# Performance work log

Hardware: AMD Instinct MI355X
Metric: run time of the kernel (lower is better)

The kernel has to match this reference:

```python
import jax, jax.numpy as jnp
import numpy as np

N_HEAD = 8
N_FEAT = 512
EPS = 1e-6


def _forward(query, Wq, bq, Wk, bk, Wv, bv, Wo, bo):
    # query: (bsz, tgt_len, E). key = value = query (self-attention).
    bsz, tgt_len, E = query.shape
    head_dim = E // N_HEAD
    n = bsz * N_HEAD

    # Faithful to torch: .view((L, N, E)) is a RESHAPE, not a transpose.
    x = query.reshape(tgt_len, bsz, E)

    q = x @ Wq.T + bq
    k = x @ Wk.T + bk
    v = x @ Wv.T + bv

    # relu activation on q, k (act_fun='relu')
    q = jax.nn.relu(q).reshape(tgt_len, n, head_dim).swapaxes(0, 1)  # (n, L, d)
    k = jax.nn.relu(k).reshape(tgt_len, n, head_dim).swapaxes(0, 1)  # (n, L, d)
    v = v.reshape(tgt_len, n, head_dim).swapaxes(0, 1)               # (n, L, d)

    # cos reweighting: weight_index = pi/2 * arange(1, m+1) / m
    m = tgt_len
    idx = (np.pi / 2) * jnp.arange(1, m + 1, dtype=query.dtype) / m  # (L,)
    idx = idx[None, :, None]                                         # (1, L, 1)
    q_ = jnp.concatenate([q * jnp.sin(idx), q * jnp.cos(idx)], axis=-1)  # (n, L, 2d)
    k_ = jnp.concatenate([k * jnp.sin(idx), k * jnp.cos(idx)], axis=-1)  # (n, L, 2d)

    # causal linear attention via cumsum recurrence
    kv = jnp.einsum('nld,nlm->nldm', k_, v)          # (n, L, 2d, d)
    kv_cum = jnp.cumsum(kv, axis=1)                  # (n, L, 2d, d)
    qkv = jnp.einsum('nld,nldm->nlm', q_, kv_cum)    # (n, L, d)
    k_cum = jnp.cumsum(k_, axis=1)                   # (n, L, 2d)
    denom = jnp.clip(jnp.einsum('nld,nld->nl', q_, k_cum), EPS, None)
    attn = qkv / denom[..., None]                    # (n, L, d)

    attn = attn.swapaxes(0, 1).reshape(tgt_len, bsz, E)
    out = attn @ Wo.T + bo
    # Faithful to torch: final .view back to (bsz, tgt_len, E) is a reshape.
    return out.reshape(bsz, tgt_len, N_FEAT)


def setup_inputs() -> dict:
    key = jax.random.key(0)
    ks = jax.random.split(key, 9)
    bsz, L, E = 2, 1024, N_FEAT
    scale = 0.02
    return {
        'query': jax.random.normal(ks[0], (bsz, L, E), dtype=jnp.float32),
        'Wq': jax.random.normal(ks[1], (E, E), dtype=jnp.float32) * scale,
        'bq': jnp.zeros((E,), dtype=jnp.float32),
        'Wk': jax.random.normal(ks[2], (E, E), dtype=jnp.float32) * scale,
        'bk': jnp.zeros((E,), dtype=jnp.float32),
        'Wv': jax.random.normal(ks[3], (E, E), dtype=jnp.float32) * scale,
        'bv': jnp.zeros((E,), dtype=jnp.float32),
        'Wo': jax.random.normal(ks[4], (E, E), dtype=jnp.float32) * scale,
        'bo': jnp.zeros((E,), dtype=jnp.float32),
    }


def reference(query, Wq, bq, Wk, bk, Wv, bv, Wo, bo):
    return _forward(query, Wq, bq, Wk, bk, Wv, bv, Wo, bo)
```

## Files before the change

kernel.cpp:

```cpp
#include <hip/hip_runtime.h>
#include <math.h>

#define LSEQ 1024
#define EDIM 512
#define HD 64
#define CCH 32
#define NCH 32
#define DFEAT 128

typedef unsigned short u16;
typedef short bf16x8 __attribute__((ext_vector_type(8)));
typedef float f32x4 __attribute__((ext_vector_type(4)));

__device__ __forceinline__ u16 f2bf(float f) {
    unsigned u = __float_as_uint(f);
    unsigned r = (u + 0x7fffu + ((u >> 16) & 1u)) >> 16;
    return (u16)r;
}
__device__ __forceinline__ float bf2f(u16 x) {
    return __uint_as_float((unsigned)x << 16);
}
__device__ __forceinline__ void async16(void* lds, const void* g) {
    __builtin_amdgcn_global_load_lds(
        (const __attribute__((address_space(1))) unsigned int*)g,
        (__attribute__((address_space(3))) unsigned int*)lds, 16, 0, 0);
}

__global__ __launch_bounds__(256) void cast_kernel(
    const float* __restrict__ X,  const float* __restrict__ Wq,
    const float* __restrict__ Wk, const float* __restrict__ Wv,
    const float* __restrict__ Wo, u16* __restrict__ Xb, u16* __restrict__ Wb)
{
    int i = blockIdx.x * 256 + threadIdx.x;
    const float* src; u16* dst; int off;
    if (i < 262144)      { src = X;  dst = Xb;          off = i; }
    else if (i < 327680) { src = Wq; dst = Wb;          off = i - 262144; }
    else if (i < 393216) { src = Wk; dst = Wb + 262144; off = i - 327680; }
    else if (i < 458752) { src = Wv; dst = Wb + 524288; off = i - 393216; }
    else                 { src = Wo; dst = Wb + 786432; off = i - 458752; }
    float4 v = *(const float4*)&src[(size_t)off * 4];
    ushort4 o; o.x = f2bf(v.x); o.y = f2bf(v.y); o.z = f2bf(v.z); o.w = f2bf(v.w);
    *(ushort4*)&dst[(size_t)off * 4] = o;
}

__global__ __launch_bounds__(256) void qkv_mfma_kernel(
    const u16* __restrict__ Xb, const u16* __restrict__ Wb,
    const float* __restrict__ bq, const float* __restrict__ bk, const float* __restrict__ bv,
    u16* __restrict__ qf, u16* __restrict__ kf, u16* __restrict__ vf)
{
    const int z = blockIdx.z;
    const u16* __restrict__ W = Wb + (size_t)z * 262144;
    const float* __restrict__ bias = (z == 0) ? bq : (z == 1) ? bk : bv;
    const int r0 = blockIdx.x * 128;
    const int j0 = blockIdx.y * 64;
    __shared__ u16 As[128 * 32];
    __shared__ u16 Bs[64 * 32];
    const int t = threadIdx.x;
    const int wave = t >> 6, lane = t & 63;
    const int cl = lane & 15, rg4 = lane >> 4;
    f32x4 acc[2][4];
    #pragma unroll
    for (int ri = 0; ri < 2; ++ri)
        #pragma unroll
        for (int cj = 0; cj < 4; ++cj) acc[ri][cj] = (f32x4){0.f, 0.f, 0.f, 0.f};

    for (int kb = 0; kb < 512; kb += 32) {
        #pragma unroll
        for (int i = 0; i < 2; ++i) {
            int chunk = i * 256 + t;
            int row = chunk >> 2, kg = chunk & 3;
            async16(&As[(i * 256 + wave * 64) * 8], Xb + (size_t)(r0 + row) * 512 + kb + kg * 8);
        }
        {
            int row = t >> 2, kg = t & 3;
            async16(&Bs[(wave * 64) * 8], W + (size_t)(j0 + row) * 512 + kb + kg * 8);
        }
        __syncthreads();
        bf16x8 af[2], bg[4];
        #pragma unroll
        for (int ri = 0; ri < 2; ++ri)
            af[ri] = *(const bf16x8*)&As[(wave * 32 + ri * 16 + cl) * 32 + rg4 * 8];
        #pragma unroll
        for (int cj = 0; cj < 4; ++cj)
            bg[cj] = *(const bf16x8*)&Bs[(cj * 16 + cl) * 32 + rg4 * 8];
        #pragma unroll
        for (int ri = 0; ri < 2; ++ri)
            #pragma unroll
            for (int cj = 0; cj < 4; ++cj)
                acc[ri][cj] = __builtin_amdgcn_mfma_f32_16x16x32_bf16(af[ri], bg[cj], acc[ri][cj], 0, 0, 0);
        __syncthreads();
    }

    float biasv[4];
    #pragma unroll
    for (int cj = 0; cj < 4; ++cj) biasv[cj] = bias[j0 + cj * 16 + cl];
    const int h = j0 >> 6;
    #pragma unroll
    for (int ri = 0; ri < 2; ++ri) {
        #pragma unroll
        for (int rr = 0; rr < 4; ++rr) {
            const int row_g = r0 + wave * 32 + ri * 16 + rg4 * 4 + rr;
            const int l = row_g >> 1, bb = row_g & 1;
            if (z < 2) {
                float ang = 1.5707963267948966f * (float)(l + 1) * (1.0f / 1024.0f);
                float sv, cv;
                sincosf(ang, &sv, &cv);
                u16* __restrict__ dst = (z == 0) ? qf : kf;
                size_t base = (size_t)((bb * 8 + h) * LSEQ + l) * DFEAT;
                #pragma unroll
                for (int cj = 0; cj < 4; ++cj) {
                    const int d = cj * 16 + cl;
                    float y = fmaxf(acc[ri][cj][rr] + biasv[cj], 0.f);
                    dst[base + d]      = f2bf(y * sv);
                    dst[base + d + 64] = f2bf(y * cv);
                }
            } else {
                size_t base = (size_t)((bb * 8 + h) * LSEQ + l) * HD;
                #pragma unroll
                for (int cj = 0; cj < 4; ++cj) {
                    const int d = cj * 16 + cl;
                    vf[base + d] = f2bf(acc[ri][cj][rr] + biasv[cj]);
                }
            }
        }
    }
}

__global__ __launch_bounds__(256) void chunk_sum_kernel(
    const u16* __restrict__ kf, const u16* __restrict__ vf,
    u16* __restrict__ KVc, float* __restrict__ K1c)
{
    const int n = blockIdx.x >> 5;
    const int c = blockIdx.x & 31;
    __shared__ u16 Ks[32 * 128];
    __shared__ u16 KT[128 * 32];
    __shared__ u16 Vs[32 * 64];
    __shared__ u16 VT[64 * 32];
    const int t = threadIdx.x;
    const int wave = t >> 6, lane = t & 63;
    const int cl = lane & 15, rg4 = lane >> 4;
    const u16* kbase = kf + (size_t)(n * LSEQ + c * CCH) * DFEAT;
    const u16* vbase = vf + (size_t)(n * LSEQ + c * CCH) * HD;
    #pragma unroll
    for (int i = 0; i < 2; ++i)
        async16(&Ks[(i * 256 + wave * 64) * 8], kbase + (size_t)(i * 256 + t) * 8);
    async16(&Vs[(wave * 64) * 8], vbase + (size_t)t * 8);
    __syncthreads();
    {
        int m = t & 63, l0 = (t >> 6) * 8;
        u16 tmp[8];
        #pragma unroll
        for (int j = 0; j < 8; ++j) tmp[j] = Vs[(l0 + j) * 64 + m];
        *(bf16x8*)&VT[m * 32 + l0] = *(bf16x8*)tmp;
    }
    {
        int d = t & 127, l0 = (t >> 7) * 16;
        #pragma unroll
        for (int half = 0; half < 2; ++half) {
            u16 tmp[8];
            #pragma unroll
            for (int j = 0; j < 8; ++j) tmp[j] = Ks[(l0 + half * 8 + j) * 128 + d];
            *(bf16x8*)&KT[d * 32 + l0 + half * 8] = *(bf16x8*)tmp;
        }
    }
    __syncthreads();
    bf16x8 af = *(const bf16x8*)&VT[(wave * 16 + cl) * 32 + rg4 * 8];
    f32x4 acc[8];
    #pragma unroll
    for (int ni = 0; ni < 8; ++ni) {
        bf16x8 bfr = *(const bf16x8*)&KT[(ni * 16 + cl) * 32 + rg4 * 8];
        acc[ni] = __builtin_amdgcn_mfma_f32_16x16x32_bf16(af, bfr, (f32x4){0.f,0.f,0.f,0.f}, 0, 0, 0);
    }
    u16* outp = KVc + (size_t)(n * NCH + c) * (HD * DFEAT);
    #pragma unroll
    for (int ni = 0; ni < 8; ++ni)
        #pragma unroll
        for (int r = 0; r < 4; ++r)
            outp[(size_t)(wave * 16 + rg4 * 4 + r) * 128 + ni * 16 + cl] = f2bf(acc[ni][r]);
    if (t < 128) {
        float s = 0.f;
        #pragma unroll
        for (int g = 0; g < 4; ++g) {
            bf16x8 kv = *(const bf16x8*)&KT[t * 32 + g * 8];
            #pragma unroll
            for (int j = 0; j < 8; ++j) s += bf2f(((u16*)&kv)[j]);
        }
        K1c[(size_t)(n * NCH + c) * DFEAT + t] = s;
    }
}

__global__ __launch_bounds__(256) void prefix_kernel(
    const u16* __restrict__ KVc, const float* __restrict__ K1c,
    u16* __restrict__ Spt, float* __restrict__ K1p)
{
    const int b = blockIdx.x, t = threadIdx.x;
    const int n = b >> 5;
    const int e = (b & 31) * 256 + t;
    const u16* src = KVc + (size_t)n * NCH * 8192 + e;
    u16* dst = Spt + (size_t)n * NCH * 8192 + e;
    float v[32];
    #pragma unroll
    for (int cc = 0; cc < 32; ++cc) v[cc] = bf2f(src[(size_t)cc * 8192]);
    float run = 0.f;
    #pragma unroll
    for (int cc = 0; cc < 32; ++cc) { dst[(size_t)cc * 8192] = f2bf(run); run += v[cc]; }
    if (b < 8) {
        const int idx = b * 256 + t;
        const int nn = idx >> 7, d = idx & 127;
        const float* s2 = K1c + (size_t)nn * NCH * DFEAT + d;
        float* d2 = K1p + (size_t)nn * NCH * DFEAT + d;
        float v2[32];
        #pragma unroll
        for (int cc = 0; cc < 32; ++cc) v2[cc] = s2[cc * DFEAT];
        float run2 = 0.f;
        #pragma unroll
        for (int cc = 0; cc < 32; ++cc) { d2[cc * DFEAT] = run2; run2 += v2[cc]; }
    }
}

__global__ __launch_bounds__(256) void attn_kernel(
    const u16* __restrict__ qf, const u16* __restrict__ kf, const u16* __restrict__ vf,
    const u16* __restrict__ Spt, const float* __restrict__ K1p,
    u16* __restrict__ Amb)
{
    const int n = blockIdx.x >> 5;
    const int c = blockIdx.x & 31;
    __shared__ u16 Qs[32 * 136];
    __shared__ u16 Ks[32 * 136];
    __shared__ u16 VT[64 * 32];
    __shared__ u16 Am[32 * 32];
    __shared__ float K1s[128];
    __shared__ float dsum2[2][32];
    __shared__ float qk1[32];
    const int t = threadIdx.x;
    const int wave = t >> 6, lane = t & 63;
    const int cl = lane & 15, rg4 = lane >> 4;
    const int mi = wave >> 1, nh = wave & 1;

    const u16* qbase = qf + (size_t)(n * LSEQ + c * CCH) * DFEAT;
    const u16* kbase = kf + (size_t)(n * LSEQ + c * CCH) * DFEAT;
    const u16* vbase = vf + (size_t)(n * LSEQ + c * CCH) * HD;
    const u16* spbase = Spt + (size_t)(n * NCH + c) * 8192;

    bf16x8 spf[2][4];
    #pragma unroll
    for (int ni2 = 0; ni2 < 2; ++ni2)
        #pragma unroll
        for (int ks = 0; ks < 4; ++ks)
            spf[ni2][ks] = *(const bf16x8*)&spbase[((2 * nh + ni2) * 16 + cl) * 128 + ks * 32 + rg4 * 8];

    #pragma unroll
    for (int i = 0; i < 2; ++i) {
        int chunk = i * 256 + t;
        int row = chunk >> 4, c8 = chunk & 15;
        *(bf16x8*)&Qs[row * 136 + c8 * 8] = *(const bf16x8*)&qbase[row * 128 + c8 * 8];
        *(bf16x8*)&Ks[row * 136 + c8 * 8] = *(const bf16x8*)&kbase[row * 128 + c8 * 8];
    }
    {
        u16 tmp[8];
        #pragma unroll
        for (int j = 0; j < 8; ++j) tmp[j] = vbase[(wave * 8 + j) * HD + lane];
        *(bf16x8*)&VT[lane * 32 + wave * 8] = *(bf16x8*)tmp;
    }
    if (t < 128) K1s[t] = K1p[(size_t)(n * NCH + c) * DFEAT + t];
    __syncthreads();

    f32x4 a_acc = (f32x4){0.f, 0.f, 0.f, 0.f};
    #pragma unroll
    for (int ks = 0; ks < 4; ++ks) {
        bf16x8 aq = *(const bf16x8*)&Qs[(mi * 16 + cl) * 136 + ks * 32 + rg4 * 8];
        bf16x8 bk = *(const bf16x8*)&Ks[(nh * 16 + cl) * 136 + ks * 32 + rg4 * 8];
        a_acc = __builtin_amdgcn_mfma_f32_16x16x32_bf16(aq, bk, a_acc, 0, 0, 0);
    }
    #pragma unroll
    for (int r = 0; r < 4; ++r) {
        int l_loc = mi * 16 + rg4 * 4 + r;
        int lp_loc = nh * 16 + cl;
        float v = (lp_loc <= l_loc) ? a_acc[r] : 0.f;
        Am[l_loc * 32 + lp_loc] = f2bf(v);
        float s = v;
        s += __shfl_xor(s, 1); s += __shfl_xor(s, 2);
        s += __shfl_xor(s, 4); s += __shfl_xor(s, 8);
        if (cl == 0) dsum2[nh][l_loc] = s;
    }
    {
        int row = wave * 8 + (lane >> 3), seg = lane & 7;
        float s = 0.f;
        #pragma unroll
        for (int j = 0; j < 16; ++j) {
            int d = seg * 16 + j;
            s += bf2f(Qs[row * 136 + d]) * K1s[d];
        }
        s += __shfl_xor(s, 1); s += __shfl_xor(s, 2); s += __shfl_xor(s, 4);
        if (seg == 0) qk1[row] = s;
    }
    __syncthreads();

    f32x4 oacc[2] = {(f32x4){0.f,0.f,0.f,0.f}, (f32x4){0.f,0.f,0.f,0.f}};
    #pragma unroll
    for (int ks = 0; ks < 4; ++ks) {
        bf16x8 aq = *(const bf16x8*)&Qs[(mi * 16 + cl) * 136 + ks * 32 + rg4 * 8];
        #pragma unroll
        for (int ni2 = 0; ni2 < 2; ++ni2)
            oacc[ni2] = __builtin_amdgcn_mfma_f32_16x16x32_bf16(aq, spf[ni2][ks], oacc[ni2], 0, 0, 0);
    }
    {
        bf16x8 aa = *(const bf16x8*)&Am[(mi * 16 + cl) * 32 + rg4 * 8];
        #pragma unroll
        for (int ni2 = 0; ni2 < 2; ++ni2) {
            bf16x8 bv = *(const bf16x8*)&VT[((2 * nh + ni2) * 16 + cl) * 32 + rg4 * 8];
            oacc[ni2] = __builtin_amdgcn_mfma_f32_16x16x32_bf16(aa, bv, oacc[ni2], 0, 0, 0);
        }
    }
    const int bb = n >> 3, h = n & 7;
    #pragma unroll
    for (int r = 0; r < 4; ++r) {
        int l_loc = mi * 16 + rg4 * 4 + r;
        float den = fmaxf(dsum2[0][l_loc] + dsum2[1][l_loc] + qk1[l_loc], 1e-6f);
        float inv = 1.0f / den;
        int rrow = (c * CCH + l_loc) * 2 + bb;
        #pragma unroll
        for (int ni2 = 0; ni2 < 2; ++ni2) {
            int m = (2 * nh + ni2) * 16 + cl;
            Amb[(size_t)rrow * EDIM + h * 64 + m] = f2bf(oacc[ni2][r] * inv);
        }
    }
}

__global__ __launch_bounds__(256) void out_mfma_kernel(
    const u16* __restrict__ Amb, const u16* __restrict__ Wob,
    const float* __restrict__ bo, float* __restrict__ out)
{
    const int r0 = blockIdx.x * 64;
    const int j0 = blockIdx.y * 64;
    __shared__ u16 As[64 * 32];
    __shared__ u16 Bs[64 * 32];
    const int t = threadIdx.x;
    const int wave = t >> 6, lane = t & 63;
    const int cl = lane & 15, rg4 = lane >> 4;
    f32x4 acc[4];
    #pragma unroll
    for (int cj = 0; cj < 4; ++cj) acc[cj] = (f32x4){0.f, 0.f, 0.f, 0.f};

    for (int kb = 0; kb < 512; kb += 32) {
        {
            int row = t >> 2, kg = t & 3;
            async16(&As[(wave * 64) * 8], Amb + (size_t)(r0 + row) * 512 + kb + kg * 8);
            async16(&Bs[(wave * 64) * 8], Wob + (size_t)(j0 + row) * 512 + kb + kg * 8);
        }
        __syncthreads();
        bf16x8 af = *(const bf16x8*)&As[(wave * 16 + cl) * 32 + rg4 * 8];
        bf16x8 bg[4];
        #pragma unroll
        for (int cj = 0; cj < 4; ++cj)
            bg[cj] = *(const bf16x8*)&Bs[(cj * 16 + cl) * 32 + rg4 * 8];
        #pragma unroll
        for (int cj = 0; cj < 4; ++cj)
            acc[cj] = __builtin_amdgcn_mfma_f32_16x16x32_bf16(af, bg[cj], acc[cj], 0, 0, 0);
        __syncthreads();
    }

    float bov[4];
    #pragma unroll
    for (int cj = 0; cj < 4; ++cj) bov[cj] = bo[j0 + cj * 16 + cl];
    #pragma unroll
    for (int rr = 0; rr < 4; ++rr) {
        const int row_g = r0 + wave * 16 + rg4 * 4 + rr;
        #pragma unroll
        for (int cj = 0; cj < 4; ++cj)
            out[(size_t)row_g * EDIM + j0 + cj * 16 + cl] = acc[cj][rr] + bov[cj];
    }
}

extern "C" void kernel_launch(void* const* d_in, const int* in_sizes, int n_in,
                              void* d_out, int out_size, void* d_ws, size_t ws_size,
                              hipStream_t stream) {
    const float* X  = (const float*)d_in[0];
    const float* Wq = (const float*)d_in[1]; const float* bq = (const float*)d_in[2];
    const float* Wk = (const float*)d_in[3]; const float* bk = (const float*)d_in[4];
    const float* Wv = (const float*)d_in[5]; const float* bv = (const float*)d_in[6];
    const float* Wo = (const float*)d_in[7]; const float* bo = (const float*)d_in[8];
    float* out = (float*)d_out;
    char* base = (char*)d_ws;
    u16*   qf  = (u16*)(base + 0);
    u16*   kf  = (u16*)(base + 4194304);
    u16*   vf  = (u16*)(base + 8388608);
    u16*   KVc = (u16*)(base + 10485760);
    float* K1c = (float*)(base + 18874368);
    u16*   Spt = (u16*)(base + 19136512);
    float* K1p = (float*)(base + 27525120);
    u16*   Amb = (u16*)(base + 27787264);
    u16*   Xb  = (u16*)(base + 29884416);
    u16*   Wb  = (u16*)(base + 31981568);

    hipLaunchKernelGGL(cast_kernel, dim3(2048), dim3(256), 0, stream,
                       X, Wq, Wk, Wv, Wo, Xb, Wb);
    hipLaunchKernelGGL(qkv_mfma_kernel, dim3(16, 8, 3), dim3(256), 0, stream,
                       Xb, Wb, bq, bk, bv, qf, kf, vf);
    hipLaunchKernelGGL(chunk_sum_kernel, dim3(512), dim3(256), 0, stream, kf, vf, KVc, K1c);
    hipLaunchKernelGGL(prefix_kernel, dim3(512), dim3(256), 0, stream, KVc, K1c, Spt, K1p);
    hipLaunchKernelGGL(attn_kernel, dim3(512), dim3(256), 0, stream,
                       qf, kf, vf, Spt, K1p, Amb);
    hipLaunchKernelGGL(out_mfma_kernel, dim3(32, 8), dim3(256), 0, stream,
                       Amb, Wb + 786432, bo, out);
}
```

Baseline: 111.0 us.

## Fuse fp32-to-bf16 cast, QKV projection and chunk KV sums into one kernel

Removes the separate cast kernel by converting fp32 X and weights to bf16 in registers while staging them into LDS, with register prefetch of the next k-slice. It computes Q, K and V together per 64-row tile and head, then reuses the K/V tile in LDS to compute per-chunk KV outer products and K sums, which eliminates the chunk_sum kernel and its reload of kf/vf. The output GEMM likewise converts Wo on the fly. This cuts two launches and several global round-trips, at the cost of a smaller grid (256 blocks) and redundant conversion of weights in every block.

```diff
diff --git a/kernel.cpp b/kernel.cpp
--- a/kernel.cpp
+++ b/kernel.cpp
@@ -1,4 +1,5 @@
 #include <hip/hip_runtime.h>
+#include <hip/hip_bf16.h>
 #include <math.h>
 
 #define LSEQ 1024
@@ -20,172 +21,165 @@
 __device__ __forceinline__ float bf2f(u16 x) {
     return __uint_as_float((unsigned)x << 16);
 }
+__device__ __forceinline__ void cvt2(float a, float b, u16& x, u16& y) {
+    float2 f; f.x = a; f.y = b;
+    __hip_bfloat162 p = __float22bfloat162_rn(f);
+    x = *reinterpret_cast<u16*>(&p.x);
+    y = *reinterpret_cast<u16*>(&p.y);
+}
+__device__ __forceinline__ bf16x8 pack8(float4 a, float4 b) {
+    u16 r[8];
+    cvt2(a.x, a.y, r[0], r[1]); cvt2(a.z, a.w, r[2], r[3]);
+    cvt2(b.x, b.y, r[4], r[5]); cvt2(b.z, b.w, r[6], r[7]);
+    return *(bf16x8*)r;
+}
 __device__ __forceinline__ void async16(void* lds, const void* g) {
     __builtin_amdgcn_global_load_lds(
         (const __attribute__((address_space(1))) unsigned int*)g,
         (__attribute__((address_space(3))) unsigned int*)lds, 16, 0, 0);
 }
 
-__global__ __launch_bounds__(256) void cast_kernel(
-    const float* __restrict__ X,  const float* __restrict__ Wq,
-    const float* __restrict__ Wk, const float* __restrict__ Wv,
-    const float* __restrict__ Wo, u16* __restrict__ Xb, u16* __restrict__ Wb)
+__global__ __launch_bounds__(256) void qkvchunk_kernel(
+    const float* __restrict__ X,
+    const float* __restrict__ Wq, const float* __restrict__ bq,
+    const float* __restrict__ Wk, const float* __restrict__ bk,
+    const float* __restrict__ Wv, const float* __restrict__ bv,
+    u16* __restrict__ qf, u16* __restrict__ kf, u16* __restrict__ vf,
+    u16* __restrict__ KVc, float* __restrict__ K1c)
 {
-    int i = blockIdx.x * 256 + threadIdx.x;
-    const float* src; u16* dst; int off;
-    if (i < 262144)      { src = X;  dst = Xb;          off = i; }
-    else if (i < 327680) { src = Wq; dst = Wb;          off = i - 262144; }
-    else if (i < 393216) { src = Wk; dst = Wb + 262144; off = i - 327680; }
-    else if (i < 458752) { src = Wv; dst = Wb + 524288; off = i - 393216; }
-    else                 { src = Wo; dst = Wb + 786432; off = i - 458752; }
-    float4 v = *(const float4*)&src[(size_t)off * 4];
-    ushort4 o; o.x = f2bf(v.x); o.y = f2bf(v.y); o.z = f2bf(v.z); o.w = f2bf(v.w);
-    *(ushort4*)&dst[(size_t)off * 4] = o;
-}
-
-__global__ __launch_bounds__(256) void qkv_mfma_kernel(
-    const u16* __restrict__ Xb, const u16* __restrict__ Wb,
-    const float* __restrict__ bq, const float* __restrict__ bk, const float* __restrict__ bv,
-    u16* __restrict__ qf, u16* __restrict__ kf, u16* __restrict__ vf)
-{
-    const int z = blockIdx.z;
-    const u16* __restrict__ W = Wb + (size_t)z * 262144;
-    const float* __restrict__ bias = (z == 0) ? bq : (z == 1) ? bk : bv;
-    const int r0 = blockIdx.x * 128;
-    const int j0 = blockIdx.y * 64;
-    __shared__ u16 As[128 * 32];
-    __shared__ u16 Bs[64 * 32];
+    __shared__ union {
+        struct { u16 As[64 * 32], Bq[64 * 32], Bk[64 * 32], Bv[64 * 32]; } p1;
+        struct { u16 KT[2 * 128 * 32], VT[2 * 64 * 32]; } p2;
+    } sh;
+    const int bx = blockIdx.x;
+    const int tile = bx >> 3, h = bx & 7;
+    const int r0 = tile * 64, j0 = h * 64;
     const int t = threadIdx.x;
     const int wave = t >> 6, lane = t & 63;
     const int cl = lane & 15, rg4 = lane >> 4;
-    f32x4 acc[2][4];
+    const int rpair = wave >> 1, half = wave & 1;
+
+    const int srow = t >> 2, sq4 = (t & 3) * 8;
+
+    f32x4 accq[2][2], acck[2][2], accv[2][2];
     #pragma unroll
     for (int ri = 0; ri < 2; ++ri)
         #pragma unroll
-        for (int cj = 0; cj < 4; ++cj) acc[ri][cj] = (f32x4){0.f, 0.f, 0.f, 0.f};
+        for (int cjl = 0; cjl < 2; ++cjl) {
+            accq[ri][cjl] = (f32x4){0.f, 0.f, 0.f, 0.f};
+            acck[ri][cjl] = (f32x4){0.f, 0.f, 0.f, 0.f};
+            accv[ri][cjl] = (f32x4){0.f, 0.f, 0.f, 0.f};
+        }
+
+    const float* xrp = X  + (size_t)(r0 + srow) * 512 + sq4;
+    const float* qrp = Wq + (size_t)(j0 + srow) * 512 + sq4;
+    const float* krp = Wk + (size_t)(j0 + srow) * 512 + sq4;
+    const float* vrp = Wv + (size_t)(j0 + srow) * 512 + sq4;
+    float4 xr0 = *(const float4*)xrp,       xr1 = *(const float4*)(xrp + 4);
+    float4 wq0 = *(const float4*)qrp,       wq1 = *(const float4*)(qrp + 4);
+    float4 wk0 = *(const float4*)krp,       wk1 = *(const float4*)(krp + 4);
+    float4 wv0 = *(const float4*)vrp,       wv1 = *(const float4*)(vrp + 4);
 
     for (int kb = 0; kb < 512; kb += 32) {
-        #pragma unroll
-        for (int i = 0; i < 2; ++i) {
-            int chunk = i * 256 + t;
-            int row = chunk >> 2, kg = chunk & 3;
-            async16(&As[(i * 256 + wave * 64) * 8], Xb + (size_t)(r0 + row) * 512 + kb + kg * 8);
-        }
-        {
-            int row = t >> 2, kg = t & 3;
-            async16(&Bs[(wave * 64) * 8], W + (size_t)(j0 + row) * 512 + kb + kg * 8);
-        }
         __syncthreads();
-        bf16x8 af[2], bg[4];
+        *(bf16x8*)&sh.p1.As[srow * 32 + sq4] = pack8(xr0, xr1);
+        *(bf16x8*)&sh.p1.Bq[srow * 32 + sq4] = pack8(wq0, wq1);
+        *(bf16x8*)&sh.p1.Bk[srow * 32 + sq4] = pack8(wk0, wk1);
+        *(bf16x8*)&sh.p1.Bv[srow * 32 + sq4] = pack8(wv0, wv1);
+        __syncthreads();
+        if (kb + 32 < 512) {
+            const float* xp = xrp + kb + 32;
+            const float* qp = qrp + kb + 32;
+            const float* kp = krp + kb + 32;
+            const float* vp = vrp + kb + 32;
+            xr0 = *(const float4*)xp; xr1 = *(const float4*)(xp + 4);
+            wq0 = *(const float4*)qp; wq1 = *(const float4*)(qp + 4);
+            wk0 = *(const float4*)kp; wk1 = *(const float4*)(kp + 4);
+            wv0 = *(const float4*)vp; wv1 = *(const float4*)(vp + 4);
+        }
+        bf16x8 af[2];
         #pragma unroll
         for (int ri = 0; ri < 2; ++ri)
-            af[ri] = *(const bf16x8*)&As[(wave * 32 + ri * 16 + cl) * 32 + rg4 * 8];
-        #pragma unroll
-        for (int cj = 0; cj < 4; ++cj)
-            bg[cj] = *(const bf16x8*)&Bs[(cj * 16 + cl) * 32 + rg4 * 8];
-        #pragma unroll
-        for (int ri = 0; ri < 2; ++ri)
+            af[ri] = *(const bf16x8*)&sh.p1.As[(rpair * 32 + ri * 16 + cl) * 32 + rg4 * 8];
+        #pragma unroll
+        for (int cjl = 0; cjl < 2; ++cjl) {
+            const int cj = half * 2 + cjl;
+            bf16x8 b1 = *(const bf16x8*)&sh.p1.Bq[(cj * 16 + cl) * 32 + rg4 * 8];
+            bf16x8 b2 = *(const bf16x8*)&sh.p1.Bk[(cj * 16 + cl) * 32 + rg4 * 8];
+            bf16x8 b3 = *(const bf16x8*)&sh.p1.Bv[(cj * 16 + cl) * 32 + rg4 * 8];
             #pragma unroll
-            for (int cj = 0; cj < 4; ++cj)
-                acc[ri][cj] = __builtin_amdgcn_mfma_f32_16x16x32_bf16(af[ri], bg[cj], acc[ri][cj], 0, 0, 0);
-        __syncthreads();
-    }
-
-    float biasv[4];
-    #pragma unroll
-    for (int cj = 0; cj < 4; ++cj) biasv[cj] = bias[j0 + cj * 16 + cl];
-    const int h = j0 >> 6;
+            for (int ri = 0; ri < 2; ++ri) {
+                accq[ri][cjl] = __builtin_amdgcn_mfma_f32_16x16x32_bf16(af[ri], b1, accq[ri][cjl], 0, 0, 0);
+                acck[ri][cjl] = __builtin_amdgcn_mfma_f32_16x16x32_bf16(af[ri], b2, acck[ri][cjl], 0, 0, 0);
+                accv[ri][cjl] = __builtin_amdgcn_mfma_f32_16x16x32_bf16(af[ri], b3, accv[ri][cjl], 0, 0, 0);
+            }
+        }
+    }
+    __syncthreads();
+
+    float bqv[2], bkv[2], bvv[2];
+    #pragma unroll
+    for (int cjl = 0; cjl < 2; ++cjl) {
+        const int jg = j0 + (half * 2 + cjl) * 16 + cl;
+        bqv[cjl] = bq[jg]; bkv[cjl] = bk[jg]; bvv[cjl] = bv[jg];
+    }
     #pragma unroll
     for (int ri = 0; ri < 2; ++ri) {
         #pragma unroll
         for (int rr = 0; rr < 4; ++rr) {
-            const int row_g = r0 + wave * 32 + ri * 16 + rg4 * 4 + rr;
-            const int l = row_g >> 1, bb = row_g & 1;
-            if (z < 2) {
-                float ang = 1.5707963267948966f * (float)(l + 1) * (1.0f / 1024.0f);
-                float sv, cv;
-                sincosf(ang, &sv, &cv);
-                u16* __restrict__ dst = (z == 0) ? qf : kf;
-                size_t base = (size_t)((bb * 8 + h) * LSEQ + l) * DFEAT;
-                #pragma unroll
-                for (int cj = 0; cj < 4; ++cj) {
-                    const int d = cj * 16 + cl;
-                    float y = fmaxf(acc[ri][cj][rr] + biasv[cj], 0.f);
-                    dst[base + d]      = f2bf(y * sv);
-                    dst[base + d + 64] = f2bf(y * cv);
-                }
-            } else {
-                size_t base = (size_t)((bb * 8 + h) * LSEQ + l) * HD;
-                #pragma unroll
-                for (int cj = 0; cj < 4; ++cj) {
-                    const int d = cj * 16 + cl;
-                    vf[base + d] = f2bf(acc[ri][cj][rr] + biasv[cj]);
-                }
+            const int row_loc = rpair * 32 + ri * 16 + rg4 * 4 + rr;
+            const int row_g = r0 + row_loc;
+            const int l = row_g >> 1, bb = row_loc & 1, lc = row_loc >> 1;
+            const int n = bb * 8 + h;
+            float ang = 1.5707963267948966f * (float)(l + 1) * (1.0f / 1024.0f);
+            float sv, cv;
+            sincosf(ang, &sv, &cv);
+            const size_t qkbase = (size_t)(n * LSEQ + l) * DFEAT;
+            const size_t vbase  = (size_t)(n * LSEQ + l) * HD;
+            #pragma unroll
+            for (int cjl = 0; cjl < 2; ++cjl) {
+                const int d = (half * 2 + cjl) * 16 + cl;
+                float yq = fmaxf(accq[ri][cjl][rr] + bqv[cjl], 0.f);
+                u16 q0, q1; cvt2(yq * sv, yq * cv, q0, q1);
+                qf[qkbase + d] = q0; qf[qkbase + d + 64] = q1;
+                float yk = fmaxf(acck[ri][cjl][rr] + bkv[cjl], 0.f);
+                u16 k0, k1; cvt2(yk * sv, yk * cv, k0, k1);
+                kf[qkbase + d] = k0; kf[qkbase + d + 64] = k1;
+                sh.p2.KT[(bb * 128 + d) * 32 + lc]      = k0;
+                sh.p2.KT[(bb * 128 + d + 64) * 32 + lc] = k1;
+                float yv = accv[ri][cjl][rr] + bvv[cjl];
+                u16 v0 = f2bf(yv);
+                vf[vbase + d] = v0;
+                sh.p2.VT[(bb * 64 + d) * 32 + lc] = v0;
             }
         }
     }
-}
-
-__global__ __launch_bounds__(256) void chunk_sum_kernel(
-    const u16* __restrict__ kf, const u16* __restrict__ vf,
-    u16* __restrict__ KVc, float* __restrict__ K1c)
-{
-    const int n = blockIdx.x >> 5;
-    const int c = blockIdx.x & 31;
-    __shared__ u16 Ks[32 * 128];
-    __shared__ u16 KT[128 * 32];
-    __shared__ u16 Vs[32 * 64];
-    __shared__ u16 VT[64 * 32];
-    const int t = threadIdx.x;
-    const int wave = t >> 6, lane = t & 63;
-    const int cl = lane & 15, rg4 = lane >> 4;
-    const u16* kbase = kf + (size_t)(n * LSEQ + c * CCH) * DFEAT;
-    const u16* vbase = vf + (size_t)(n * LSEQ + c * CCH) * HD;
-    #pragma unroll
-    for (int i = 0; i < 2; ++i)
-        async16(&Ks[(i * 256 + wave * 64) * 8], kbase + (size_t)(i * 256 + t) * 8);
-    async16(&Vs[(wave * 64) * 8], vbase + (size_t)t * 8);
     __syncthreads();
+
+    #pragma unroll
+    for (int bb2 = 0; bb2 < 2; ++bb2) {
+        bf16x8 af2 = *(const bf16x8*)&sh.p2.VT[(bb2 * 64 + wave * 16 + cl) * 32 + rg4 * 8];
+        const int n2 = bb2 * 8 + h;
+        u16* kvout = KVc + (size_t)(n2 * NCH + tile) * (HD * DFEAT);
+        #pragma unroll
+        for (int dt = 0; dt < 8; ++dt) {
+            bf16x8 bf2 = *(const bf16x8*)&sh.p2.KT[(bb2 * 128 + dt * 16 + cl) * 32 + rg4 * 8];
+            f32x4 a2 = __builtin_amdgcn_mfma_f32_16x16x32_bf16(af2, bf2, (f32x4){0.f,0.f,0.f,0.f}, 0, 0, 0);
+            #pragma unroll
+            for (int rr = 0; rr < 4; ++rr)
+                kvout[(size_t)(wave * 16 + rg4 * 4 + rr) * 128 + dt * 16 + cl] = f2bf(a2[rr]);
+        }
+    }
     {
-        int m = t & 63, l0 = (t >> 6) * 8;
-        u16 tmp[8];
-        #pragma unroll
-        for (int j = 0; j < 8; ++j) tmp[j] = Vs[(l0 + j) * 64 + m];
-        *(bf16x8*)&VT[m * 32 + l0] = *(bf16x8*)tmp;
-    }
-    {
-        int d = t & 127, l0 = (t >> 7) * 16;
-        #pragma unroll
-        for (int half = 0; half < 2; ++half) {
-            u16 tmp[8];
-            #pragma unroll
-            for (int j = 0; j < 8; ++j) tmp[j] = Ks[(l0 + half * 8 + j) * 128 + d];
-            *(bf16x8*)&KT[d * 32 + l0 + half * 8] = *(bf16x8*)tmp;
-        }
-    }
-    __syncthreads();
-    bf16x8 af = *(const bf16x8*)&VT[(wave * 16 + cl) * 32 + rg4 * 8];
-    f32x4 acc[8];
-    #pragma unroll
-    for (int ni = 0; ni < 8; ++ni) {
-        bf16x8 bfr = *(const bf16x8*)&KT[(ni * 16 + cl) * 32 + rg4 * 8];
-        acc[ni] = __builtin_amdgcn_mfma_f32_16x16x32_bf16(af, bfr, (f32x4){0.f,0.f,0.f,0.f}, 0, 0, 0);
-    }
-    u16* outp = KVc + (size_t)(n * NCH + c) * (HD * DFEAT);
-    #pragma unroll
-    for (int ni = 0; ni < 8; ++ni)
-        #pragma unroll
-        for (int r = 0; r < 4; ++r)
-            outp[(size_t)(wave * 16 + rg4 * 4 + r) * 128 + ni * 16 + cl] = f2bf(acc[ni][r]);
-    if (t < 128) {
+        const int bbk = t >> 7, dk = t & 127;
         float s = 0.f;
         #pragma unroll
         for (int g = 0; g < 4; ++g) {
-            bf16x8 kv = *(const bf16x8*)&KT[t * 32 + g * 8];
+            bf16x8 kv = *(const bf16x8*)&sh.p2.KT[(bbk * 128 + dk) * 32 + g * 8];
             #pragma unroll
             for (int j = 0; j < 8; ++j) s += bf2f(((u16*)&kv)[j]);
         }
-        K1c[(size_t)(n * NCH + c) * DFEAT + t] = s;
+        K1c[(size_t)((bbk * 8 + h) * NCH + tile) * DFEAT + dk] = s;
     }
 }
 
@@ -328,7 +322,7 @@
 }
 
 __global__ __launch_bounds__(256) void out_mfma_kernel(
-    const u16* __restrict__ Amb, const u16* __restrict__ Wob,
+    const u16* __restrict__ Amb, const float* __restrict__ Wo,
     const float* __restrict__ bo, float* __restrict__ out)
 {
     const int r0 = blockIdx.x * 64;
@@ -338,26 +332,29 @@
     const int t = threadIdx.x;
     const int wave = t >> 6, lane = t & 63;
     const int cl = lane & 15, rg4 = lane >> 4;
+    const int srow = t >> 2, sq4 = (t & 3) * 8;
     f32x4 acc[4];
     #pragma unroll
     for (int cj = 0; cj < 4; ++cj) acc[cj] = (f32x4){0.f, 0.f, 0.f, 0.f};
 
+    const float* wop = Wo + (size_t)(j0 + srow) * 512 + sq4;
+    float4 w0 = *(const float4*)wop, w1 = *(const float4*)(wop + 4);
+
     for (int kb = 0; kb < 512; kb += 32) {
-        {
-            int row = t >> 2, kg = t & 3;
-            async16(&As[(wave * 64) * 8], Amb + (size_t)(r0 + row) * 512 + kb + kg * 8);
-            async16(&Bs[(wave * 64) * 8], Wob + (size_t)(j0 + row) * 512 + kb + kg * 8);
-        }
         __syncthreads();
+        async16(&As[(wave * 64) * 8], Amb + (size_t)(r0 + (t >> 2)) * 512 + kb + (t & 3) * 8);
+        *(bf16x8*)&Bs[srow * 32 + sq4] = pack8(w0, w1);
+        __syncthreads();
+        if (kb + 32 < 512) {
+            const float* p = wop + kb + 32;
+            w0 = *(const float4*)p; w1 = *(const float4*)(p + 4);
+        }
         bf16x8 af = *(const bf16x8*)&As[(wave * 16 + cl) * 32 + rg4 * 8];
-        bf16x8 bg[4];
-        #pragma unroll
-        for (int cj = 0; cj < 4; ++cj)
-            bg[cj] = *(const bf16x8*)&Bs[(cj * 16 + cl) * 32 + rg4 * 8];
-        #pragma unroll
-        for (int cj = 0; cj < 4; ++cj)
-            acc[cj] = __builtin_amdgcn_mfma_f32_16x16x32_bf16(af, bg[cj], acc[cj], 0, 0, 0);
-        __syncthreads();
+        #pragma unroll
+        for (int cj = 0; cj < 4; ++cj) {
+            bf16x8 bg = *(const bf16x8*)&Bs[(cj * 16 + cl) * 32 + rg4 * 8];
+            acc[cj] = __builtin_amdgcn_mfma_f32_16x16x32_bf16(af, bg, acc[cj], 0, 0, 0);
+        }
     }
 
     float bov[4];
@@ -390,17 +387,12 @@
     u16*   Spt = (u16*)(base + 19136512);
     float* K1p = (float*)(base + 27525120);
     u16*   Amb = (u16*)(base + 27787264);
-    u16*   Xb  = (u16*)(base + 29884416);
-    u16*   Wb  = (u16*)(base + 31981568);
-
-    hipLaunchKernelGGL(cast_kernel, dim3(2048), dim3(256), 0, stream,
-                       X, Wq, Wk, Wv, Wo, Xb, Wb);
-    hipLaunchKernelGGL(qkv_mfma_kernel, dim3(16, 8, 3), dim3(256), 0, stream,
-                       Xb, Wb, bq, bk, bv, qf, kf, vf);
-    hipLaunchKernelGGL(chunk_sum_kernel, dim3(512), dim3(256), 0, stream, kf, vf, KVc, K1c);
+
+    hipLaunchKernelGGL(qkvchunk_kernel, dim3(256), dim3(256), 0, stream,
+                       X, Wq, bq, Wk, bk, Wv, bv, qf, kf, vf, KVc, K1c);
     hipLaunchKernelGGL(prefix_kernel, dim3(512), dim3(256), 0, stream, KVc, K1c, Spt, K1p);
     hipLaunchKernelGGL(attn_kernel, dim3(512), dim3(256), 0, stream,
                        qf, kf, vf, Spt, K1p, Amb);
     hipLaunchKernelGGL(out_mfma_kernel, dim3(32, 8), dim3(256), 0, stream,
-                       Amb, Wb + 786432, bo, out);
-}
+                       Amb, Wo, bo, out);
+}
```

Measured after the change: 113.9 us. +2.7%, slower.

## Double causal chunk size to 64, halving chunk-state traffic

Applied to the files above, without the earlier changes.

Raises the chunk length of the chunked causal linear attention from 32 to 64 tokens, so there are 16 chunks per head instead of 32. The chunk-sum, prefix and attention kernels are rewritten for the larger tiles: each wave now covers 16 full rows with 4 column tiles, and LDS arrays are padded. The goal is to halve the per-chunk KV state written, scanned and reread, at the cost of fewer blocks (256), more intra-chunk MFMA work and more registers per thread.

```diff
diff --git a/kernel.cpp b/kernel.cpp
--- a/kernel.cpp
+++ b/kernel.cpp
@@ -4,8 +4,8 @@
 #define LSEQ 1024
 #define EDIM 512
 #define HD 64
-#define CCH 32
-#define NCH 32
+#define CCH 64
+#define NCH 16
 #define DFEAT 128
 
 typedef unsigned short u16;
@@ -130,58 +130,67 @@
     const u16* __restrict__ kf, const u16* __restrict__ vf,
     u16* __restrict__ KVc, float* __restrict__ K1c)
 {
-    const int n = blockIdx.x >> 5;
-    const int c = blockIdx.x & 31;
-    __shared__ u16 Ks[32 * 128];
-    __shared__ u16 KT[128 * 32];
-    __shared__ u16 Vs[32 * 64];
-    __shared__ u16 VT[64 * 32];
+    const int n = blockIdx.x >> 4;
+    const int c = blockIdx.x & 15;
+    __shared__ u16 Ks[64 * 128];
+    __shared__ u16 KT[128 * 68];
+    __shared__ u16 Vs[64 * 64];
+    __shared__ u16 VT[64 * 68];
     const int t = threadIdx.x;
     const int wave = t >> 6, lane = t & 63;
     const int cl = lane & 15, rg4 = lane >> 4;
     const u16* kbase = kf + (size_t)(n * LSEQ + c * CCH) * DFEAT;
     const u16* vbase = vf + (size_t)(n * LSEQ + c * CCH) * HD;
     #pragma unroll
+    for (int i = 0; i < 4; ++i)
+        async16(&Ks[(i * 256 + wave * 64) * 8], kbase + (size_t)(i * 256 + t) * 8);
+    #pragma unroll
     for (int i = 0; i < 2; ++i)
-        async16(&Ks[(i * 256 + wave * 64) * 8], kbase + (size_t)(i * 256 + t) * 8);
-    async16(&Vs[(wave * 64) * 8], vbase + (size_t)t * 8);
+        async16(&Vs[(i * 256 + wave * 64) * 8], vbase + (size_t)(i * 256 + t) * 8);
     __syncthreads();
     {
-        int m = t & 63, l0 = (t >> 6) * 8;
-        u16 tmp[8];
-        #pragma unroll
-        for (int j = 0; j < 8; ++j) tmp[j] = Vs[(l0 + j) * 64 + m];
-        *(bf16x8*)&VT[m * 32 + l0] = *(bf16x8*)tmp;
-    }
-    {
-        int d = t & 127, l0 = (t >> 7) * 16;
+        int m = t & 63, l0 = (t >> 6) * 16;
         #pragma unroll
         for (int half = 0; half < 2; ++half) {
             u16 tmp[8];
             #pragma unroll
-            for (int j = 0; j < 8; ++j) tmp[j] = Ks[(l0 + half * 8 + j) * 128 + d];
-            *(bf16x8*)&KT[d * 32 + l0 + half * 8] = *(bf16x8*)tmp;
+            for (int j = 0; j < 8; ++j) tmp[j] = Vs[(l0 + half * 8 + j) * 64 + m];
+            *(bf16x8*)&VT[m * 68 + l0 + half * 8] = *(bf16x8*)tmp;
+        }
+    }
+    {
+        int d = t & 127, l0 = (t >> 7) * 32;
+        #pragma unroll
+        for (int q = 0; q < 4; ++q) {
+            u16 tmp[8];
+            #pragma unroll
+            for (int j = 0; j < 8; ++j) tmp[j] = Ks[(l0 + q * 8 + j) * 128 + d];
+            *(bf16x8*)&KT[d * 68 + l0 + q * 8] = *(bf16x8*)tmp;
         }
     }
     __syncthreads();
-    bf16x8 af = *(const bf16x8*)&VT[(wave * 16 + cl) * 32 + rg4 * 8];
-    f32x4 acc[8];
-    #pragma unroll
-    for (int ni = 0; ni < 8; ++ni) {
-        bf16x8 bfr = *(const bf16x8*)&KT[(ni * 16 + cl) * 32 + rg4 * 8];
-        acc[ni] = __builtin_amdgcn_mfma_f32_16x16x32_bf16(af, bfr, (f32x4){0.f,0.f,0.f,0.f}, 0, 0, 0);
-    }
-    u16* outp = KVc + (size_t)(n * NCH + c) * (HD * DFEAT);
-    #pragma unroll
-    for (int ni = 0; ni < 8; ++ni)
+    bf16x8 af[2];
+    #pragma unroll
+    for (int ks = 0; ks < 2; ++ks)
+        af[ks] = *(const bf16x8*)&VT[(wave * 16 + cl) * 68 + ks * 32 + rg4 * 8];
+    u16* kvout = KVc + (size_t)(n * NCH + c) * (HD * DFEAT);
+    #pragma unroll
+    for (int dt = 0; dt < 8; ++dt) {
+        f32x4 acc = (f32x4){0.f, 0.f, 0.f, 0.f};
+        #pragma unroll
+        for (int ks = 0; ks < 2; ++ks) {
+            bf16x8 bfr = *(const bf16x8*)&KT[(dt * 16 + cl) * 68 + ks * 32 + rg4 * 8];
+            acc = __builtin_amdgcn_mfma_f32_16x16x32_bf16(af[ks], bfr, acc, 0, 0, 0);
+        }
         #pragma unroll
         for (int r = 0; r < 4; ++r)
-            outp[(size_t)(wave * 16 + rg4 * 4 + r) * 128 + ni * 16 + cl] = f2bf(acc[ni][r]);
+            kvout[(size_t)(wave * 16 + rg4 * 4 + r) * 128 + dt * 16 + cl] = f2bf(acc[r]);
+    }
     if (t < 128) {
         float s = 0.f;
         #pragma unroll
-        for (int g = 0; g < 4; ++g) {
-            bf16x8 kv = *(const bf16x8*)&KT[t * 32 + g * 8];
+        for (int g = 0; g < 8; ++g) {
+            bf16x8 kv = *(const bf16x8*)&KT[t * 68 + g * 8];
             #pragma unroll
             for (int j = 0; j < 8; ++j) s += bf2f(((u16*)&kv)[j]);
         }
@@ -198,23 +207,23 @@
     const int e = (b & 31) * 256 + t;
     const u16* src = KVc + (size_t)n * NCH * 8192 + e;
     u16* dst = Spt + (size_t)n * NCH * 8192 + e;
-    float v[32];
-    #pragma unroll
-    for (int cc = 0; cc < 32; ++cc) v[cc] = bf2f(src[(size_t)cc * 8192]);
+    float v[NCH];
+    #pragma unroll
+    for (int cc = 0; cc < NCH; ++cc) v[cc] = bf2f(src[(size_t)cc * 8192]);
     float run = 0.f;
     #pragma unroll
-    for (int cc = 0; cc < 32; ++cc) { dst[(size_t)cc * 8192] = f2bf(run); run += v[cc]; }
+    for (int cc = 0; cc < NCH; ++cc) { dst[(size_t)cc * 8192] = f2bf(run); run += v[cc]; }
     if (b < 8) {
         const int idx = b * 256 + t;
         const int nn = idx >> 7, d = idx & 127;
         const float* s2 = K1c + (size_t)nn * NCH * DFEAT + d;
         float* d2 = K1p + (size_t)nn * NCH * DFEAT + d;
-        float v2[32];
-        #pragma unroll
-        for (int cc = 0; cc < 32; ++cc) v2[cc] = s2[cc * DFEAT];
+        float v2[NCH];
+        #pragma unroll
+        for (int cc = 0; cc < NCH; ++cc) v2[cc] = s2[cc * DFEAT];
         float run2 = 0.f;
         #pragma unroll
-        for (int cc = 0; cc < 32; ++cc) { d2[cc * DFEAT] = run2; run2 += v2[cc]; }
+        for (int cc = 0; cc < NCH; ++cc) { d2[cc * DFEAT] = run2; run2 += v2[cc]; }
     }
 }
 
@@ -223,106 +232,120 @@
     const u16* __restrict__ Spt, const float* __restrict__ K1p,
     u16* __restrict__ Amb)
 {
-    const int n = blockIdx.x >> 5;
-    const int c = blockIdx.x & 31;
-    __shared__ u16 Qs[32 * 136];
-    __shared__ u16 Ks[32 * 136];
-    __shared__ u16 VT[64 * 32];
-    __shared__ u16 Am[32 * 32];
+    const int n = blockIdx.x >> 4;
+    const int c = blockIdx.x & 15;
+    __shared__ u16 Qs[64 * 136];
+    __shared__ u16 Ks[64 * 136];
+    __shared__ u16 VT[64 * 68];
+    __shared__ u16 Am[64 * 68];
     __shared__ float K1s[128];
-    __shared__ float dsum2[2][32];
-    __shared__ float qk1[32];
+    __shared__ float dsum[64];
+    __shared__ float qk1[64];
     const int t = threadIdx.x;
     const int wave = t >> 6, lane = t & 63;
     const int cl = lane & 15, rg4 = lane >> 4;
-    const int mi = wave >> 1, nh = wave & 1;
 
     const u16* qbase = qf + (size_t)(n * LSEQ + c * CCH) * DFEAT;
     const u16* kbase = kf + (size_t)(n * LSEQ + c * CCH) * DFEAT;
     const u16* vbase = vf + (size_t)(n * LSEQ + c * CCH) * HD;
     const u16* spbase = Spt + (size_t)(n * NCH + c) * 8192;
 
-    bf16x8 spf[2][4];
-    #pragma unroll
-    for (int ni2 = 0; ni2 < 2; ++ni2)
+    bf16x8 spf[4][4];
+    #pragma unroll
+    for (int nj = 0; nj < 4; ++nj)
         #pragma unroll
         for (int ks = 0; ks < 4; ++ks)
-            spf[ni2][ks] = *(const bf16x8*)&spbase[((2 * nh + ni2) * 16 + cl) * 128 + ks * 32 + rg4 * 8];
-
-    #pragma unroll
-    for (int i = 0; i < 2; ++i) {
+            spf[nj][ks] = *(const bf16x8*)&spbase[(nj * 16 + cl) * 128 + ks * 32 + rg4 * 8];
+
+    #pragma unroll
+    for (int i = 0; i < 4; ++i) {
         int chunk = i * 256 + t;
         int row = chunk >> 4, c8 = chunk & 15;
         *(bf16x8*)&Qs[row * 136 + c8 * 8] = *(const bf16x8*)&qbase[row * 128 + c8 * 8];
         *(bf16x8*)&Ks[row * 136 + c8 * 8] = *(const bf16x8*)&kbase[row * 128 + c8 * 8];
     }
     {
-        u16 tmp[8];
-        #pragma unroll
-        for (int j = 0; j < 8; ++j) tmp[j] = vbase[(wave * 8 + j) * HD + lane];
-        *(bf16x8*)&VT[lane * 32 + wave * 8] = *(bf16x8*)tmp;
+        #pragma unroll
+        for (int half = 0; half < 2; ++half) {
+            u16 tmp[8];
+            #pragma unroll
+            for (int j = 0; j < 8; ++j) tmp[j] = vbase[(wave * 16 + half * 8 + j) * HD + lane];
+            *(bf16x8*)&VT[lane * 68 + wave * 16 + half * 8] = *(bf16x8*)tmp;
+        }
     }
     if (t < 128) K1s[t] = K1p[(size_t)(n * NCH + c) * DFEAT + t];
     __syncthreads();
 
-    f32x4 a_acc = (f32x4){0.f, 0.f, 0.f, 0.f};
+    f32x4 a_acc[4];
+    #pragma unroll
+    for (int nj = 0; nj < 4; ++nj) a_acc[nj] = (f32x4){0.f, 0.f, 0.f, 0.f};
     #pragma unroll
     for (int ks = 0; ks < 4; ++ks) {
-        bf16x8 aq = *(const bf16x8*)&Qs[(mi * 16 + cl) * 136 + ks * 32 + rg4 * 8];
-        bf16x8 bk = *(const bf16x8*)&Ks[(nh * 16 + cl) * 136 + ks * 32 + rg4 * 8];
-        a_acc = __builtin_amdgcn_mfma_f32_16x16x32_bf16(aq, bk, a_acc, 0, 0, 0);
+        bf16x8 aq = *(const bf16x8*)&Qs[(wave * 16 + cl) * 136 + ks * 32 + rg4 * 8];
+        #pragma unroll
+        for (int nj = 0; nj < 4; ++nj) {
+            bf16x8 bk = *(const bf16x8*)&Ks[(nj * 16 + cl) * 136 + ks * 32 + rg4 * 8];
+            a_acc[nj] = __builtin_amdgcn_mfma_f32_16x16x32_bf16(aq, bk, a_acc[nj], 0, 0, 0);
+        }
     }
     #pragma unroll
     for (int r = 0; r < 4; ++r) {
-        int l_loc = mi * 16 + rg4 * 4 + r;
-        int lp_loc = nh * 16 + cl;
-        float v = (lp_loc <= l_loc) ? a_acc[r] : 0.f;
-        Am[l_loc * 32 + lp_loc] = f2bf(v);
-        float s = v;
+        int l_loc = wave * 16 + rg4 * 4 + r;
+        float rs = 0.f;
+        #pragma unroll
+        for (int nj = 0; nj < 4; ++nj) {
+            int lp = nj * 16 + cl;
+            float v = (lp <= l_loc) ? a_acc[nj][r] : 0.f;
+            Am[l_loc * 68 + lp] = f2bf(v);
+            rs += v;
+        }
+        rs += __shfl_xor(rs, 1); rs += __shfl_xor(rs, 2);
+        rs += __shfl_xor(rs, 4); rs += __shfl_xor(rs, 8);
+        if (cl == 0) dsum[l_loc] = rs;
+    }
+    {
+        int row = wave * 16 + (lane >> 2), seg = lane & 3;
+        float s = 0.f;
+        #pragma unroll
+        for (int j = 0; j < 32; ++j) {
+            int d = seg * 32 + j;
+            s += bf2f(Qs[row * 136 + d]) * K1s[d];
+        }
         s += __shfl_xor(s, 1); s += __shfl_xor(s, 2);
-        s += __shfl_xor(s, 4); s += __shfl_xor(s, 8);
-        if (cl == 0) dsum2[nh][l_loc] = s;
-    }
-    {
-        int row = wave * 8 + (lane >> 3), seg = lane & 7;
-        float s = 0.f;
-        #pragma unroll
-        for (int j = 0; j < 16; ++j) {
-            int d = seg * 16 + j;
-            s += bf2f(Qs[row * 136 + d]) * K1s[d];
-        }
-        s += __shfl_xor(s, 1); s += __shfl_xor(s, 2); s += __shfl_xor(s, 4);
         if (seg == 0) qk1[row] = s;
     }
     __syncthreads();
 
-    f32x4 oacc[2] = {(f32x4){0.f,0.f,0.f,0.f}, (f32x4){0.f,0.f,0.f,0.f}};
+    f32x4 oacc[4];
+    #pragma unroll
+    for (int nj = 0; nj < 4; ++nj) oacc[nj] = (f32x4){0.f, 0.f, 0.f, 0.f};
     #pragma unroll
     for (int ks = 0; ks < 4; ++ks) {
-        bf16x8 aq = *(const bf16x8*)&Qs[(mi * 16 + cl) * 136 + ks * 32 + rg4 * 8];
-        #pragma unroll
-        for (int ni2 = 0; ni2 < 2; ++ni2)
-            oacc[ni2] = __builtin_amdgcn_mfma_f32_16x16x32_bf16(aq, spf[ni2][ks], oacc[ni2], 0, 0, 0);
-    }
-    {
-        bf16x8 aa = *(const bf16x8*)&Am[(mi * 16 + cl) * 32 + rg4 * 8];
-        #pragma unroll
-        for (int ni2 = 0; ni2 < 2; ++ni2) {
-            bf16x8 bv = *(const bf16x8*)&VT[((2 * nh + ni2) * 16 + cl) * 32 + rg4 * 8];
-            oacc[ni2] = __builtin_amdgcn_mfma_f32_16x16x32_bf16(aa, bv, oacc[ni2], 0, 0, 0);
+        bf16x8 aq = *(const bf16x8*)&Qs[(wave * 16 + cl) * 136 + ks * 32 + rg4 * 8];
+        #pragma unroll
+        for (int nj = 0; nj < 4; ++nj)
+            oacc[nj] = __builtin_amdgcn_mfma_f32_16x16x32_bf16(aq, spf[nj][ks], oacc[nj], 0, 0, 0);
+    }
+    #pragma unroll
+    for (int ks2 = 0; ks2 < 2; ++ks2) {
+        bf16x8 aa = *(const bf16x8*)&Am[(wave * 16 + cl) * 68 + ks2 * 32 + rg4 * 8];
+        #pragma unroll
+        for (int nj = 0; nj < 4; ++nj) {
+            bf16x8 bv = *(const bf16x8*)&VT[(nj * 16 + cl) * 68 + ks2 * 32 + rg4 * 8];
+            oacc[nj] = __builtin_amdgcn_mfma_f32_16x16x32_bf16(aa, bv, oacc[nj], 0, 0, 0);
         }
     }
     const int bb = n >> 3, h = n & 7;
     #pragma unroll
     for (int r = 0; r < 4; ++r) {
-        int l_loc = mi * 16 + rg4 * 4 + r;
-        float den = fmaxf(dsum2[0][l_loc] + dsum2[1][l_loc] + qk1[l_loc], 1e-6f);
+        int l_loc = wave * 16 + rg4 * 4 + r;
+        float den = fmaxf(dsum[l_loc] + qk1[l_loc], 1e-6f);
         float inv = 1.0f / den;
         int rrow = (c * CCH + l_loc) * 2 + bb;
         #pragma unroll
-        for (int ni2 = 0; ni2 < 2; ++ni2) {
-            int m = (2 * nh + ni2) * 16 + cl;
-            Amb[(size_t)rrow * EDIM + h * 64 + m] = f2bf(oacc[ni2][r] * inv);
+        for (int nj = 0; nj < 4; ++nj) {
+            int m = nj * 16 + cl;
+            Amb[(size_t)rrow * EDIM + h * 64 + m] = f2bf(oacc[nj][r] * inv);
         }
     }
 }
@@ -386,20 +409,20 @@
     u16*   kf  = (u16*)(base + 4194304);
     u16*   vf  = (u16*)(base + 8388608);
     u16*   KVc = (u16*)(base + 10485760);
-    float* K1c = (float*)(base + 18874368);
-    u16*   Spt = (u16*)(base + 19136512);
-    float* K1p = (float*)(base + 27525120);
-    u16*   Amb = (u16*)(base + 27787264);
-    u16*   Xb  = (u16*)(base + 29884416);
-    u16*   Wb  = (u16*)(base + 31981568);
+    float* K1c = (float*)(base + 14680064);
+    u16*   Spt = (u16*)(base + 14811136);
+    float* K1p = (float*)(base + 19005440);
+    u16*   Amb = (u16*)(base + 19136512);
+    u16*   Xb  = (u16*)(base + 21233664);
+    u16*   Wb  = (u16*)(base + 23330816);
 
     hipLaunchKernelGGL(cast_kernel, dim3(2048), dim3(256), 0, stream,
                        X, Wq, Wk, Wv, Wo, Xb, Wb);
     hipLaunchKernelGGL(qkv_mfma_kernel, dim3(16, 8, 3), dim3(256), 0, stream,
                        Xb, Wb, bq, bk, bv, qf, kf, vf);
-    hipLaunchKernelGGL(chunk_sum_kernel, dim3(512), dim3(256), 0, stream, kf, vf, KVc, K1c);
+    hipLaunchKernelGGL(chunk_sum_kernel, dim3(256), dim3(256), 0, stream, kf, vf, KVc, K1c);
     hipLaunchKernelGGL(prefix_kernel, dim3(512), dim3(256), 0, stream, KVc, K1c, Spt, K1p);
-    hipLaunchKernelGGL(attn_kernel, dim3(512), dim3(256), 0, stream,
+    hipLaunchKernelGGL(attn_kernel, dim3(256), dim3(256), 0, stream,
                        qf, kf, vf, Spt, K1p, Amb);
     hipLaunchKernelGGL(out_mfma_kernel, dim3(32, 8), dim3(256), 0, stream,
                        Amb, Wb + 786432, bo, out);
```

Measured after the change: 110.1 us, median of 2. No clear change (-0.7%).
